# Kernel tuning notes

Measured on AMD Instinct MI355X. Metric: run time of the kernel, lower is better.

The kernel has to match this reference:

```python
import jax, jax.numpy as jnp
import numpy as np

IN_C, OUT_C, SCALE, S, NF = 2, 2, 2, 3, 64
MODES = 3
NB = IN_C * MODES  # one sub-module per (input channel, mode)
PAD = S - 1


def _pixel_shuffle(x, r):
    n, c, h, w = x.shape
    oc = c // (r * r)
    x = x.reshape(n, oc, r, r, h, w).transpose(0, 1, 4, 2, 5, 3)
    return x.reshape(n, oc, h * r, w * r)


def _round_ste(x):
    # straight-through round: forward = round(x), backward = identity
    return x + jax.lax.stop_gradient(jnp.round(x) - x)


def _branch(xin, w1, b1, w2, b2, w3, b3, w4, b4, w5, b5, w6, b6):
    # xin: [4B, 2, H+PAD, W+PAD]; tiny SxS conv then dense 1x1 chain (MuLUT unit)
    y = jax.lax.conv_general_dilated(xin, w1, (1, 1), 'VALID',
                                     dimension_numbers=('NCHW', 'OIHW', 'NCHW'))
    y = jax.nn.relu(y + b1[None, :, None, None])

    def dense(t, w, b):
        f = jax.nn.relu(jnp.einsum('bchw,oc->bohw', t, w) + b[None, :, None, None])
        return jnp.concatenate([t, f], axis=1)

    y = dense(y, w2, b2)
    y = dense(y, w3, b3)
    y = dense(y, w4, b4)
    y = dense(y, w5, b5)
    return jnp.einsum('bchw,oc->bohw', y, w6) + b6[None, :, None, None]


def _forward(x, prev_x, W1, B1, W2, B2, W3, B3, W4, B4, W5, B5, W6, B6):
    B, _, H, W = x.shape

    def prep(c):
        # rotating x and prev_x jointly == rotating each separately (elementwise pairing preserved)
        xc = jnp.concatenate([x[:, c:c + 1], prev_x[:, c:c + 1]], axis=1)  # [B,2,H,W]
        rs = jnp.concatenate([jnp.rot90(xc, k=r, axes=(2, 3)) for r in range(4)], axis=0)  # [4B,2,H,W]
        return jnp.pad(rs, ((0, 0), (0, 0), (0, PAD), (0, PAD)), mode='edge')  # replicate pad right/bottom

    xs = jnp.stack([prep(c) for c in range(IN_C)])           # [IN_C,4B,2,Hp,Wp]
    xb = xs[np.repeat(np.arange(IN_C), MODES)]               # [NB,4B,2,Hp,Wp]
    y = jax.vmap(_branch)(xb, W1, B1, W2, B2, W3, B3, W4, B4, W5, B5, W6, B6)  # [NB,4B,OC*sc^2,H,W]
    y = jax.vmap(lambda t: _pixel_shuffle(t, SCALE))(y)      # [NB,4B,OC,sH,sW]
    y = y.reshape(NB, 4, B, OUT_C, SCALE * H, SCALE * W)
    y = jnp.stack([jnp.rot90(y[:, r], k=(4 - r) % 4, axes=(3, 4)) for r in range(4)], axis=1)
    y = _round_ste(jnp.tanh(y) * 127.0)
    # sum over rotations and modes per channel, then over channels; divide by in_c (output_quant=False)
    return y.sum(axis=(0, 1)) / IN_C


def setup_inputs():
    key = jax.random.key(0)
    ks = jax.random.split(key, 8)
    B, H = 2, 64

    def w(k, shape, fan_in):
        return jax.random.normal(k, shape, jnp.float32) * np.float32(np.sqrt(2.0 / fan_in))

    return {
        'x': jax.random.uniform(ks[0], (B, IN_C, H, H), jnp.float32),
        'prev_x': jax.random.uniform(ks[1], (B, IN_C, H, H), jnp.float32),
        'W1': w(ks[2], (NB, NF, 2, S, S), 2 * S * S), 'B1': jnp.zeros((NB, NF), jnp.float32),
        'W2': w(ks[3], (NB, NF, NF), NF), 'B2': jnp.zeros((NB, NF), jnp.float32),
        'W3': w(ks[4], (NB, NF, 2 * NF), 2 * NF), 'B3': jnp.zeros((NB, NF), jnp.float32),
        'W4': w(ks[5], (NB, NF, 3 * NF), 3 * NF), 'B4': jnp.zeros((NB, NF), jnp.float32),
        'W5': w(ks[6], (NB, NF, 4 * NF), 4 * NF), 'B5': jnp.zeros((NB, NF), jnp.float32),
        'W6': w(ks[7], (NB, OUT_C * SCALE * SCALE, 5 * NF), 5 * NF),
        'B6': jnp.zeros((NB, OUT_C * SCALE * SCALE), jnp.float32),
    }


def reference(x, prev_x, W1, B1, W2, B2, W3, B3, W4, B4, W5, B5, W6, B6):
    return _forward(x, prev_x, W1, B1, W2, B2, W3, B3, W4, B4, W5, B5, W6, B6)
```

## Files before the change

kernel.cpp:

```cpp
#include <hip/hip_runtime.h>
#include <math.h>


typedef short bf16x8 __attribute__((ext_vector_type(8)));
typedef float f32x4  __attribute__((ext_vector_type(4)));

__device__ __forceinline__ short f2bf_bits(float v) {
    union { float f; unsigned u; } x; x.f = v;
    unsigned r = x.u + 0x7FFFu + ((x.u >> 16) & 1u);
    return (short)(r >> 16);
}
__device__ __forceinline__ float bf2f(short s) {
    union { unsigned u; float f; } x; x.u = ((unsigned)(unsigned short)s) << 16;
    return x.f;
}

__global__ void prep_weights(const float* __restrict__ W1, const float* __restrict__ W2,
                             const float* __restrict__ W3, const float* __restrict__ W4,
                             const float* __restrict__ W5, const float* __restrict__ W6,
                             short* __restrict__ wsw, float* __restrict__ w1p)
{
    if (blockIdx.x < 135) {
        const int t = blockIdx.x * 256 + threadIdx.x;
        const int frag = t >> 6, lane = t & 63;
        const int b = frag / 90, slot = frag % 90;
        const int kqh = lane >> 4, rowl = lane & 15;
        const float* src; int K, kb, m; bool head = false;
        if (slot < 8)       { src = W2; K = 64;  kb = slot >> 2;        m = slot & 3; }
        else if (slot < 24) { src = W3; K = 128; kb = (slot - 8) >> 2;  m = slot & 3; }
        else if (slot < 48) { src = W4; K = 192; kb = (slot - 24) >> 2; m = slot & 3; }
        else if (slot < 80) { src = W5; K = 256; kb = (slot - 48) >> 2; m = slot & 3; }
        else                { src = W6; K = 320; kb = slot - 80; m = 0; head = true; }
        short* hi = wsw + (size_t)b * 92160 + slot * 1024 + (lane << 3);
        short* lo = hi + 512;
        #pragma unroll
        for (int j = 0; j < 8; ++j) {
            const int k = kb * 32 + ((j & 4) ? 16 : 0) + kqh * 4 + (j & 3);
            float v;
            if (!head) v = src[(size_t)(b * 64 + m * 16 + rowl) * K + k];
            else       v = (rowl < 8) ? src[(size_t)(b * 8 + rowl) * 320 + k] : 0.0f;
            const short h = f2bf_bits(v);
            hi[j] = h;
            lo[j] = f2bf_bits(v - bf2f(h));
        }
    } else {
        for (int d = threadIdx.x; d < 6912; d += 256) {
            const int bq = d / 288, rem = d % 288;
            const int it2 = rem >> 4, s16 = (rem >> 2) & 3, tt = rem & 3;
            const int b = bq >> 2, kq = bq & 3;
            const int img = it2 / 9, tap = it2 % 9;
            w1p[d] = W1[(size_t)((b * 64 + s16 * 16 + kq * 4 + tt) * 2 + img) * 9 + tap];
        }
    }
}

__device__ __forceinline__ void pack_kb(const f32x4 a, const f32x4 bq,
                                        bf16x8* ph, bf16x8* pl) {
    bf16x8 h, l;
    #pragma unroll
    for (int e = 0; e < 4; ++e) {
        float v = fmaxf(a[e], 0.0f);
        short hs = f2bf_bits(v);
        h[e] = hs; l[e] = f2bf_bits(v - bf2f(hs));
        float v2 = fmaxf(bq[e], 0.0f);
        short hs2 = f2bf_bits(v2);
        h[4 + e] = hs2; l[4 + e] = f2bf_bits(v2 - bf2f(hs2));
    }
    *ph = h; *pl = l;
}

#define ASM_VMCNT(N) asm volatile("s_waitcnt vmcnt(" #N ")" ::: "memory")

#define DENSE_STAGE(KB_IN, SLOT0, BIAS, OUTKB)                                          \
  {                                                                                      \
    f32x4 sacc[2][4];                                                                    \
    _Pragma("unroll") for (int p = 0; p < 2; ++p)                                        \
      _Pragma("unroll") for (int m = 0; m < 4; ++m)                                      \
        _Pragma("unroll") for (int rr = 0; rr < 4; ++rr)                                 \
          sacc[p][m][rr] = BIAS[m * 4 + rr];                                             \
    _Pragma("unroll") for (int kb = 0; kb < KB_IN; ++kb) {                               \
      _Pragma("unroll") for (int m = 0; m < 4; ++m) {                                    \
        const int so = (SLOT0 + kb * 4 + m) * 1024 + lane8;                              \
        bf16x8 ah = *(const bf16x8*)&wlds[so];                                           \
        bf16x8 al = *(const bf16x8*)&wlds[so + 512];                                     \
        _Pragma("unroll") for (int p = 0; p < 2; ++p) {                                  \
          sacc[p][m] = __builtin_amdgcn_mfma_f32_16x16x32_bf16(ah, act_h[p][kb], sacc[p][m], 0, 0, 0); \
          sacc[p][m] = __builtin_amdgcn_mfma_f32_16x16x32_bf16(ah, act_l[p][kb], sacc[p][m], 0, 0, 0); \
          sacc[p][m] = __builtin_amdgcn_mfma_f32_16x16x32_bf16(al, act_h[p][kb], sacc[p][m], 0, 0, 0); \
        }                                                                                \
      }                                                                                  \
    }                                                                                    \
    _Pragma("unroll") for (int p = 0; p < 2; ++p) {                                      \
      pack_kb(sacc[p][0], sacc[p][1], &act_h[p][OUTKB], &act_l[p][OUTKB]);               \
      pack_kb(sacc[p][2], sacc[p][3], &act_h[p][OUTKB + 1], &act_l[p][OUTKB + 1]);       \
    }                                                                                    \
  }

__global__ __launch_bounds__(512, 2) void mulut_main(
    const float* __restrict__ x, const float* __restrict__ px_,
    const float* __restrict__ B1, const float* __restrict__ B2,
    const float* __restrict__ B3, const float* __restrict__ B4,
    const float* __restrict__ B5, const float* __restrict__ B6,
    const short* __restrict__ wsw, const float* __restrict__ w1p,
    float* __restrict__ out)
{
    __shared__ short wlds[81920];

    const int blk = blockIdx.x;
    const int q   = blk & 15;
    const int n   = (blk >> 4) & 7;
    const int b   = blk >> 7;
    const int c   = (b >= 3) ? 1 : 0;
    const int r   = n >> 1;
    const int batch = n & 1;

    const int tid  = threadIdx.x;
    const int w    = tid >> 6;
    const int lane = tid & 63;
    const int col  = lane & 15;
    const int kq   = lane >> 4;
    const int lane8 = lane << 3;

    const int row   = q * 4 + (w >> 1);
    const int cbase = (w & 1) * 32;

    const char* wsb = (const char*)(wsw + (size_t)b * 92160);

    bf16x8 act_h[2][10];
    bf16x8 act_l[2][10];

    float bC[16], bS1[16], bS2[16], bS3[16], bS4[16], bH[4];
    #pragma unroll
    for (int i = 0; i < 16; ++i) {
        const int m = i >> 2, rr = i & 3;
        const int ch = m * 16 + kq * 4 + rr;
        bC[i]  = B1[b * 64 + ch];
        bS1[i] = B2[b * 64 + ch];
        bS2[i] = B3[b * 64 + ch];
        bS3[i] = B4[b * 64 + ch];
        bS4[i] = B5[b * 64 + ch];
    }
    #pragma unroll
    for (int rr = 0; rr < 4; ++rr) {
        const int ch = kq * 4 + rr;
        const float t = B6[b * 8 + min(ch, 7)];
        bH[rr] = (ch < 8) ? t : 0.0f;
    }

    const float* img_[2] = { x   + ((batch * 2 + c) << 12),
                             px_ + ((batch * 2 + c) << 12) };
    float g[2][2][9];
    #pragma unroll
    for (int p = 0; p < 2; ++p) {
        const int c0 = cbase + p * 16 + col;
        #pragma unroll
        for (int di = 0; di < 3; ++di) {
            const int ii = min(row + di, 63);
            #pragma unroll
            for (int dj = 0; dj < 3; ++dj) {
                const int jj = min(c0 + dj, 63);
                int si, sj;
                if      (r == 0) { si = ii;      sj = jj;      }
                else if (r == 1) { si = jj;      sj = 63 - ii; }
                else if (r == 2) { si = 63 - ii; sj = 63 - jj; }
                else             { si = 63 - jj; sj = ii;      }
                g[p][0][di * 3 + dj] = img_[0][si * 64 + sj];
                g[p][1][di * 3 + dj] = img_[1][si * 64 + sj];
            }
        }
    }

    f32x4 accc[2][4];
    #pragma unroll
    for (int p = 0; p < 2; ++p)
        #pragma unroll
        for (int s16 = 0; s16 < 4; ++s16)
            #pragma unroll
            for (int t = 0; t < 4; ++t)
                accc[p][s16][t] = bC[s16 * 4 + t];

    const f32x4* wp0 = (const f32x4*)&w1p[(b * 4 + kq) * 288];
    #pragma unroll
    for (int it = 0; it < 18; ++it) {
        const int img = it / 9, tap = it % 9;
        const float gv0 = g[0][img][tap];
        const float gv1 = g[1][img][tap];
        #pragma unroll
        for (int s16 = 0; s16 < 4; ++s16) {
            const f32x4 w4 = wp0[it * 4 + s16];
            #pragma unroll
            for (int t = 0; t < 4; ++t) {
                accc[0][s16][t] = fmaf(gv0, w4[t], accc[0][s16][t]);
                accc[1][s16][t] = fmaf(gv1, w4[t], accc[1][s16][t]);
            }
        }
    }
    #pragma unroll
    for (int p = 0; p < 2; ++p) {
        pack_kb(accc[p][0], accc[p][1], &act_h[p][0], &act_l[p][0]);
        pack_kb(accc[p][2], accc[p][3], &act_h[p][1], &act_l[p][1]);
    }

    __builtin_amdgcn_sched_barrier(0);

    #pragma unroll
    for (int ck = 0; ck < 20; ++ck) {
        const unsigned off = ck * 8192 + w * 1024;
        __builtin_amdgcn_global_load_lds((const unsigned*)(wsb + off + lane * 16),
                                         (unsigned*)&wlds[off >> 1], 16, 0, 0);
    }
    __builtin_amdgcn_sched_barrier(0);

    ASM_VMCNT(18);
    __builtin_amdgcn_s_barrier();
    DENSE_STAGE(2, 0, bS1, 2)

    ASM_VMCNT(14);
    __builtin_amdgcn_s_barrier();
    DENSE_STAGE(4, 8, bS2, 4)

    __builtin_amdgcn_s_barrier();
    #pragma unroll
    for (int hk = 0; hk < 2; ++hk) {
        const unsigned loff = hk * 8192 + w * 1024;
        __builtin_amdgcn_global_load_lds((const unsigned*)(wsb + 163840 + loff + lane * 16),
                                         (unsigned*)&wlds[loff >> 1], 16, 0, 0);
    }
    #pragma unroll
    for (int hk = 0; hk < 2; ++hk) {
        const unsigned loff = 16384 + hk * 2048 + w * 256;
        __builtin_amdgcn_global_load_lds((const unsigned*)(wsb + 163840 + loff + lane * 4),
                                         (unsigned*)&wlds[loff >> 1], 4, 0, 0);
    }
    __builtin_amdgcn_sched_barrier(0);

    ASM_VMCNT(12);
    __builtin_amdgcn_s_barrier();
    DENSE_STAGE(6, 24, bS3, 6)

    ASM_VMCNT(4);
    __builtin_amdgcn_s_barrier();
    DENSE_STAGE(8, 48, bS4, 8)

    ASM_VMCNT(0);
    __builtin_amdgcn_s_barrier();

    f32x4 hacc[2];
    #pragma unroll
    for (int p = 0; p < 2; ++p)
        #pragma unroll
        for (int rr = 0; rr < 4; ++rr)
            hacc[p][rr] = bH[rr];
    #pragma unroll
    for (int kb = 0; kb < 10; ++kb) {
        const int so = kb * 1024 + lane8;
        bf16x8 ah = *(const bf16x8*)&wlds[so];
        bf16x8 al = *(const bf16x8*)&wlds[so + 512];
        #pragma unroll
        for (int p = 0; p < 2; ++p) {
            hacc[p] = __builtin_amdgcn_mfma_f32_16x16x32_bf16(ah, act_h[p][kb], hacc[p], 0, 0, 0);
            hacc[p] = __builtin_amdgcn_mfma_f32_16x16x32_bf16(ah, act_l[p][kb], hacc[p], 0, 0, 0);
            hacc[p] = __builtin_amdgcn_mfma_f32_16x16x32_bf16(al, act_h[p][kb], hacc[p], 0, 0, 0);
        }
    }

    #pragma unroll
    for (int p = 0; p < 2; ++p) {
        const int colp = cbase + p * 16 + col;
        #pragma unroll
        for (int rr = 0; rr < 4; ++rr) {
            const int ch = kq * 4 + rr;
            if (ch < 8) {
                const int oc = ch >> 2;
                const int a  = (ch >> 1) & 1;
                const int bb = ch & 1;
                const int ip = 2 * row + a;
                const int jp = 2 * colp + bb;
                int I, J;
                if      (r == 0) { I = ip;       J = jp;       }
                else if (r == 1) { I = jp;       J = 127 - ip; }
                else if (r == 2) { I = 127 - ip; J = 127 - jp; }
                else             { I = 127 - jp; J = ip;       }
                const float v = rintf(tanhf(hacc[p][rr]) * 127.0f);
                atomicAdd(out + (((batch * 2 + oc) << 14) + I * 128 + J), v * 0.5f);
            }
        }
    }
}

extern "C" void kernel_launch(void* const* d_in, const int* in_sizes, int n_in,
                              void* d_out, int out_size, void* d_ws, size_t ws_size,
                              hipStream_t stream) {
    const float* x   = (const float*)d_in[0];
    const float* pxv = (const float*)d_in[1];
    const float* W1  = (const float*)d_in[2];
    const float* B1  = (const float*)d_in[3];
    const float* W2  = (const float*)d_in[4];
    const float* B2  = (const float*)d_in[5];
    const float* W3  = (const float*)d_in[6];
    const float* B3  = (const float*)d_in[7];
    const float* W4  = (const float*)d_in[8];
    const float* B4  = (const float*)d_in[9];
    const float* W5  = (const float*)d_in[10];
    const float* B5  = (const float*)d_in[11];
    const float* W6  = (const float*)d_in[12];
    const float* B6  = (const float*)d_in[13];
    float* out = (float*)d_out;

    short* wsw = (short*)d_ws;
    float* w1p = (float*)(wsw + 6 * 92160);

    hipMemsetAsync(out, 0, (size_t)out_size * sizeof(float), stream);
    prep_weights<<<dim3(136), dim3(256), 0, stream>>>(W1, W2, W3, W4, W5, W6, wsw, w1p);
    mulut_main<<<dim3(768), dim3(512), 0, stream>>>(
        x, pxv, B1, B2, B3, B4, B5, B6, wsw, w1p, out);
}
```

Before: 184.7 us.

## Use 1024-thread blocks with one pixel tile per wave and fold output zeroing into prep

Each block now runs 16 waves that each own a single 16-pixel column tile instead of two. This halves per-thread activation registers and drops the precomputed bias arrays, which are now read on the fly with a kq select. Weight staging into LDS uses fewer, larger chunks because more waves take part, and the vmcnt waits are adjusted to match. The output memset is folded into the prep kernel as extra zeroing blocks, removing one launch. The trade-off is less weight-fragment reuse per LDS read, since each wave now serves one tile, and occupancy depends on the compiler's register allocation at 1024 threads.

```diff
diff --git a/kernel.cpp b/kernel.cpp
--- a/kernel.cpp
+++ b/kernel.cpp
@@ -3,6 +3,7 @@
 
 
 typedef short bf16x8 __attribute__((ext_vector_type(8)));
+typedef short short4v __attribute__((ext_vector_type(4)));
 typedef float f32x4  __attribute__((ext_vector_type(4)));
 
 __device__ __forceinline__ short f2bf_bits(float v) {
@@ -18,7 +19,8 @@
 __global__ void prep_weights(const float* __restrict__ W1, const float* __restrict__ W2,
                              const float* __restrict__ W3, const float* __restrict__ W4,
                              const float* __restrict__ W5, const float* __restrict__ W6,
-                             short* __restrict__ wsw, float* __restrict__ w1p)
+                             short* __restrict__ wsw, float* __restrict__ w1p,
+                             float* __restrict__ outz)
 {
     if (blockIdx.x < 135) {
         const int t = blockIdx.x * 256 + threadIdx.x;
@@ -43,7 +45,7 @@
             hi[j] = h;
             lo[j] = f2bf_bits(v - bf2f(h));
         }
-    } else {
+    } else if (blockIdx.x == 135) {
         for (int d = threadIdx.x; d < 6912; d += 256) {
             const int bq = d / 288, rem = d % 288;
             const int it2 = rem >> 4, s16 = (rem >> 2) & 3, tt = rem & 3;
@@ -51,6 +53,11 @@
             const int img = it2 / 9, tap = it2 % 9;
             w1p[d] = W1[(size_t)((b * 64 + s16 * 16 + kq * 4 + tt) * 2 + img) * 9 + tap];
         }
+    } else {
+        const int i = ((blockIdx.x - 136) * 256 + (int)threadIdx.x) * 8;
+        f32x4 z = {0.f, 0.f, 0.f, 0.f};
+        *(f32x4*)(outz + i)     = z;
+        *(f32x4*)(outz + i + 4) = z;
     }
 }
 
@@ -69,34 +76,38 @@
     *ph = h; *pl = l;
 }
 
+__device__ __forceinline__ float sel4(int kq, const float* __restrict__ p) {
+    const float b0 = p[0], b1 = p[4], b2 = p[8], b3 = p[12];
+    const float lo = (kq & 1) ? b1 : b0;
+    const float hi = (kq & 1) ? b3 : b2;
+    return (kq & 2) ? hi : lo;
+}
+
 #define ASM_VMCNT(N) asm volatile("s_waitcnt vmcnt(" #N ")" ::: "memory")
 
-#define DENSE_STAGE(KB_IN, SLOT0, BIAS, OUTKB)                                          \
+#define DENSE_STAGE(KB_IN, SLOT0, BPTR, OUTKB)                                          \
   {                                                                                      \
-    f32x4 sacc[2][4];                                                                    \
-    _Pragma("unroll") for (int p = 0; p < 2; ++p)                                        \
-      _Pragma("unroll") for (int m = 0; m < 4; ++m)                                      \
-        _Pragma("unroll") for (int rr = 0; rr < 4; ++rr)                                 \
-          sacc[p][m][rr] = BIAS[m * 4 + rr];                                             \
+    f32x4 sacc[4];                                                                       \
+    _Pragma("unroll") for (int m = 0; m < 4; ++m)                                        \
+      _Pragma("unroll") for (int rr = 0; rr < 4; ++rr) sacc[m][rr] = 0.f;                \
     _Pragma("unroll") for (int kb = 0; kb < KB_IN; ++kb) {                               \
       _Pragma("unroll") for (int m = 0; m < 4; ++m) {                                    \
         const int so = (SLOT0 + kb * 4 + m) * 1024 + lane8;                              \
         bf16x8 ah = *(const bf16x8*)&wlds[so];                                           \
         bf16x8 al = *(const bf16x8*)&wlds[so + 512];                                     \
-        _Pragma("unroll") for (int p = 0; p < 2; ++p) {                                  \
-          sacc[p][m] = __builtin_amdgcn_mfma_f32_16x16x32_bf16(ah, act_h[p][kb], sacc[p][m], 0, 0, 0); \
-          sacc[p][m] = __builtin_amdgcn_mfma_f32_16x16x32_bf16(ah, act_l[p][kb], sacc[p][m], 0, 0, 0); \
-          sacc[p][m] = __builtin_amdgcn_mfma_f32_16x16x32_bf16(al, act_h[p][kb], sacc[p][m], 0, 0, 0); \
-        }                                                                                \
+        sacc[m] = __builtin_amdgcn_mfma_f32_16x16x32_bf16(ah, act_h[kb], sacc[m], 0, 0, 0); \
+        sacc[m] = __builtin_amdgcn_mfma_f32_16x16x32_bf16(ah, act_l[kb], sacc[m], 0, 0, 0); \
+        sacc[m] = __builtin_amdgcn_mfma_f32_16x16x32_bf16(al, act_h[kb], sacc[m], 0, 0, 0); \
       }                                                                                  \
     }                                                                                    \
-    _Pragma("unroll") for (int p = 0; p < 2; ++p) {                                      \
-      pack_kb(sacc[p][0], sacc[p][1], &act_h[p][OUTKB], &act_l[p][OUTKB]);               \
-      pack_kb(sacc[p][2], sacc[p][3], &act_h[p][OUTKB + 1], &act_l[p][OUTKB + 1]);       \
-    }                                                                                    \
+    _Pragma("unroll") for (int m = 0; m < 4; ++m)                                        \
+      _Pragma("unroll") for (int rr = 0; rr < 4; ++rr)                                   \
+        sacc[m][rr] += sel4(kq, BPTR + m * 16 + rr);                                     \
+    pack_kb(sacc[0], sacc[1], &act_h[OUTKB], &act_l[OUTKB]);                             \
+    pack_kb(sacc[2], sacc[3], &act_h[OUTKB + 1], &act_l[OUTKB + 1]);                     \
   }
 
-__global__ __launch_bounds__(512, 2) void mulut_main(
+__global__ __launch_bounds__(1024) void mulut_main(
     const float* __restrict__ x, const float* __restrict__ px_,
     const float* __restrict__ B1, const float* __restrict__ B2,
     const float* __restrict__ B3, const float* __restrict__ B4,
@@ -114,176 +125,143 @@
     const int r   = n >> 1;
     const int batch = n & 1;
 
-    const int tid  = threadIdx.x;
-    const int w    = tid >> 6;
-    const int lane = tid & 63;
-    const int col  = lane & 15;
-    const int kq   = lane >> 4;
+    const int tid   = threadIdx.x;
+    const int w     = tid >> 6;
+    const int lane  = tid & 63;
+    const int col   = lane & 15;
+    const int kq    = lane >> 4;
     const int lane8 = lane << 3;
 
-    const int row   = q * 4 + (w >> 1);
-    const int cbase = (w & 1) * 32;
+    const int row = q * 4 + (w >> 2);
+    const int px  = (w & 3) * 16 + col;
 
     const char* wsb = (const char*)(wsw + (size_t)b * 92160);
 
-    bf16x8 act_h[2][10];
-    bf16x8 act_l[2][10];
-
-    float bC[16], bS1[16], bS2[16], bS3[16], bS4[16], bH[4];
-    #pragma unroll
-    for (int i = 0; i < 16; ++i) {
-        const int m = i >> 2, rr = i & 3;
-        const int ch = m * 16 + kq * 4 + rr;
-        bC[i]  = B1[b * 64 + ch];
-        bS1[i] = B2[b * 64 + ch];
-        bS2[i] = B3[b * 64 + ch];
-        bS3[i] = B4[b * 64 + ch];
-        bS4[i] = B5[b * 64 + ch];
-    }
-    #pragma unroll
-    for (int rr = 0; rr < 4; ++rr) {
-        const int ch = kq * 4 + rr;
-        const float t = B6[b * 8 + min(ch, 7)];
-        bH[rr] = (ch < 8) ? t : 0.0f;
-    }
-
-    const float* img_[2] = { x   + ((batch * 2 + c) << 12),
-                             px_ + ((batch * 2 + c) << 12) };
-    float g[2][2][9];
-    #pragma unroll
-    for (int p = 0; p < 2; ++p) {
-        const int c0 = cbase + p * 16 + col;
+    bf16x8 act_h[10];
+    bf16x8 act_l[10];
+
+    {
+        const float* img0 = x   + ((batch * 2 + c) << 12);
+        const float* img1 = px_ + ((batch * 2 + c) << 12);
+        float g[2][9];
         #pragma unroll
         for (int di = 0; di < 3; ++di) {
             const int ii = min(row + di, 63);
             #pragma unroll
             for (int dj = 0; dj < 3; ++dj) {
-                const int jj = min(c0 + dj, 63);
+                const int jj = min(px + dj, 63);
                 int si, sj;
                 if      (r == 0) { si = ii;      sj = jj;      }
                 else if (r == 1) { si = jj;      sj = 63 - ii; }
                 else if (r == 2) { si = 63 - ii; sj = 63 - jj; }
                 else             { si = 63 - jj; sj = ii;      }
-                g[p][0][di * 3 + dj] = img_[0][si * 64 + sj];
-                g[p][1][di * 3 + dj] = img_[1][si * 64 + sj];
+                g[0][di * 3 + dj] = img0[si * 64 + sj];
+                g[1][di * 3 + dj] = img1[si * 64 + sj];
             }
         }
-    }
-
-    f32x4 accc[2][4];
-    #pragma unroll
-    for (int p = 0; p < 2; ++p)
+
+        f32x4 accc[4];
         #pragma unroll
         for (int s16 = 0; s16 < 4; ++s16)
             #pragma unroll
-            for (int t = 0; t < 4; ++t)
-                accc[p][s16][t] = bC[s16 * 4 + t];
-
-    const f32x4* wp0 = (const f32x4*)&w1p[(b * 4 + kq) * 288];
-    #pragma unroll
-    for (int it = 0; it < 18; ++it) {
-        const int img = it / 9, tap = it % 9;
-        const float gv0 = g[0][img][tap];
-        const float gv1 = g[1][img][tap];
-        #pragma unroll
-        for (int s16 = 0; s16 < 4; ++s16) {
-            const f32x4 w4 = wp0[it * 4 + s16];
-            #pragma unroll
-            for (int t = 0; t < 4; ++t) {
-                accc[0][s16][t] = fmaf(gv0, w4[t], accc[0][s16][t]);
-                accc[1][s16][t] = fmaf(gv1, w4[t], accc[1][s16][t]);
+            for (int t = 0; t < 4; ++t) accc[s16][t] = 0.f;
+
+        const f32x4* wp0 = (const f32x4*)&w1p[(b * 4 + kq) * 288];
+        #pragma unroll
+        for (int it = 0; it < 18; ++it) {
+            const float gv = g[it / 9][it % 9];
+            #pragma unroll
+            for (int s16 = 0; s16 < 4; ++s16) {
+                const f32x4 w4 = wp0[it * 4 + s16];
+                #pragma unroll
+                for (int t = 0; t < 4; ++t)
+                    accc[s16][t] = fmaf(gv, w4[t], accc[s16][t]);
             }
         }
-    }
-    #pragma unroll
-    for (int p = 0; p < 2; ++p) {
-        pack_kb(accc[p][0], accc[p][1], &act_h[p][0], &act_l[p][0]);
-        pack_kb(accc[p][2], accc[p][3], &act_h[p][1], &act_l[p][1]);
+        #pragma unroll
+        for (int m = 0; m < 4; ++m)
+            #pragma unroll
+            for (int rr = 0; rr < 4; ++rr)
+                accc[m][rr] += sel4(kq, B1 + b * 64 + m * 16 + rr);
+        pack_kb(accc[0], accc[1], &act_h[0], &act_l[0]);
+        pack_kb(accc[2], accc[3], &act_h[1], &act_l[1]);
     }
 
     __builtin_amdgcn_sched_barrier(0);
 
     #pragma unroll
-    for (int ck = 0; ck < 20; ++ck) {
-        const unsigned off = ck * 8192 + w * 1024;
+    for (int ck = 0; ck < 10; ++ck) {
+        const unsigned off = ck * 16384 + w * 1024;
         __builtin_amdgcn_global_load_lds((const unsigned*)(wsb + off + lane * 16),
                                          (unsigned*)&wlds[off >> 1], 16, 0, 0);
     }
     __builtin_amdgcn_sched_barrier(0);
 
-    ASM_VMCNT(18);
-    __builtin_amdgcn_s_barrier();
-    DENSE_STAGE(2, 0, bS1, 2)
-
-    ASM_VMCNT(14);
-    __builtin_amdgcn_s_barrier();
-    DENSE_STAGE(4, 8, bS2, 4)
-
-    __builtin_amdgcn_s_barrier();
-    #pragma unroll
-    for (int hk = 0; hk < 2; ++hk) {
-        const unsigned loff = hk * 8192 + w * 1024;
-        __builtin_amdgcn_global_load_lds((const unsigned*)(wsb + 163840 + loff + lane * 16),
-                                         (unsigned*)&wlds[loff >> 1], 16, 0, 0);
-    }
-    #pragma unroll
-    for (int hk = 0; hk < 2; ++hk) {
-        const unsigned loff = 16384 + hk * 2048 + w * 256;
-        __builtin_amdgcn_global_load_lds((const unsigned*)(wsb + 163840 + loff + lane * 4),
-                                         (unsigned*)&wlds[loff >> 1], 4, 0, 0);
+    ASM_VMCNT(9);
+    __builtin_amdgcn_s_barrier();
+    DENSE_STAGE(2, 0, B2 + b * 64, 2)
+
+    ASM_VMCNT(7);
+    __builtin_amdgcn_s_barrier();
+    DENSE_STAGE(4, 8, B3 + b * 64, 4)
+
+    __builtin_amdgcn_s_barrier();
+    {
+        const unsigned l0 = w * 1024;
+        __builtin_amdgcn_global_load_lds((const unsigned*)(wsb + 163840 + l0 + lane * 16),
+                                         (unsigned*)&wlds[l0 >> 1], 16, 0, 0);
+        const unsigned l1 = 16384 + w * 256;
+        __builtin_amdgcn_global_load_lds((const unsigned*)(wsb + 163840 + l1 + lane * 4),
+                                         (unsigned*)&wlds[l1 >> 1], 4, 0, 0);
     }
     __builtin_amdgcn_sched_barrier(0);
 
-    ASM_VMCNT(12);
-    __builtin_amdgcn_s_barrier();
-    DENSE_STAGE(6, 24, bS3, 6)
-
-    ASM_VMCNT(4);
-    __builtin_amdgcn_s_barrier();
-    DENSE_STAGE(8, 48, bS4, 8)
+    ASM_VMCNT(6);
+    __builtin_amdgcn_s_barrier();
+    DENSE_STAGE(6, 24, B4 + b * 64, 6)
+
+    ASM_VMCNT(2);
+    __builtin_amdgcn_s_barrier();
+    DENSE_STAGE(8, 48, B5 + b * 64, 8)
 
     ASM_VMCNT(0);
     __builtin_amdgcn_s_barrier();
 
-    f32x4 hacc[2];
-    #pragma unroll
-    for (int p = 0; p < 2; ++p)
-        #pragma unroll
-        for (int rr = 0; rr < 4; ++rr)
-            hacc[p][rr] = bH[rr];
+    f32x4 hacc;
+    #pragma unroll
+    for (int rr = 0; rr < 4; ++rr) hacc[rr] = 0.f;
     #pragma unroll
     for (int kb = 0; kb < 10; ++kb) {
         const int so = kb * 1024 + lane8;
         bf16x8 ah = *(const bf16x8*)&wlds[so];
         bf16x8 al = *(const bf16x8*)&wlds[so + 512];
-        #pragma unroll
-        for (int p = 0; p < 2; ++p) {
-            hacc[p] = __builtin_amdgcn_mfma_f32_16x16x32_bf16(ah, act_h[p][kb], hacc[p], 0, 0, 0);
-            hacc[p] = __builtin_amdgcn_mfma_f32_16x16x32_bf16(ah, act_l[p][kb], hacc[p], 0, 0, 0);
-            hacc[p] = __builtin_amdgcn_mfma_f32_16x16x32_bf16(al, act_h[p][kb], hacc[p], 0, 0, 0);
-        }
-    }
-
-    #pragma unroll
-    for (int p = 0; p < 2; ++p) {
-        const int colp = cbase + p * 16 + col;
-        #pragma unroll
-        for (int rr = 0; rr < 4; ++rr) {
-            const int ch = kq * 4 + rr;
-            if (ch < 8) {
-                const int oc = ch >> 2;
-                const int a  = (ch >> 1) & 1;
-                const int bb = ch & 1;
-                const int ip = 2 * row + a;
-                const int jp = 2 * colp + bb;
-                int I, J;
-                if      (r == 0) { I = ip;       J = jp;       }
-                else if (r == 1) { I = jp;       J = 127 - ip; }
-                else if (r == 2) { I = 127 - ip; J = 127 - jp; }
-                else             { I = 127 - jp; J = ip;       }
-                const float v = rintf(tanhf(hacc[p][rr]) * 127.0f);
-                atomicAdd(out + (((batch * 2 + oc) << 14) + I * 128 + J), v * 0.5f);
-            }
+        hacc = __builtin_amdgcn_mfma_f32_16x16x32_bf16(ah, act_h[kb], hacc, 0, 0, 0);
+        hacc = __builtin_amdgcn_mfma_f32_16x16x32_bf16(ah, act_l[kb], hacc, 0, 0, 0);
+        hacc = __builtin_amdgcn_mfma_f32_16x16x32_bf16(al, act_h[kb], hacc, 0, 0, 0);
+    }
+    #pragma unroll
+    for (int rr = 0; rr < 4; ++rr) {
+        const float h0 = B6[b * 8 + rr];
+        const float h1 = B6[b * 8 + 4 + rr];
+        hacc[rr] += (kq == 0) ? h0 : ((kq == 1) ? h1 : 0.f);
+    }
+
+    #pragma unroll
+    for (int rr = 0; rr < 4; ++rr) {
+        const int ch = kq * 4 + rr;
+        if (ch < 8) {
+            const int oc = ch >> 2;
+            const int a  = (ch >> 1) & 1;
+            const int bb = ch & 1;
+            const int ip = 2 * row + a;
+            const int jp = 2 * px + bb;
+            int I, J;
+            if      (r == 0) { I = ip;       J = jp;       }
+            else if (r == 1) { I = jp;       J = 127 - ip; }
+            else if (r == 2) { I = 127 - ip; J = 127 - jp; }
+            else             { I = 127 - jp; J = ip;       }
+            const float v = rintf(tanhf(hacc[rr]) * 127.0f);
+            atomicAdd(out + (((batch * 2 + oc) << 14) + I * 128 + J), v * 0.5f);
         }
     }
 }
@@ -310,8 +288,8 @@
     short* wsw = (short*)d_ws;
     float* w1p = (float*)(wsw + 6 * 92160);
 
-    hipMemsetAsync(out, 0, (size_t)out_size * sizeof(float), stream);
-    prep_weights<<<dim3(136), dim3(256), 0, stream>>>(W1, W2, W3, W4, W5, W6, wsw, w1p);
-    mulut_main<<<dim3(768), dim3(512), 0, stream>>>(
+    prep_weights<<<dim3(168), dim3(256), 0, stream>>>(W1, W2, W3, W4, W5, W6,
+                                                      wsw, w1p, out);
+    mulut_main<<<dim3(768), dim3(1024), 0, stream>>>(
         x, pxv, B1, B2, B3, B4, B5, B6, wsw, w1p, out);
 }
```

Measured after the change: 206.3 us. +11.7%, slower.
